# Optimization experiments

Measured on AMD Instinct MI355X. Metric: run time of the kernel, lower is better.

## Reference

```python
import jax, jax.numpy as jnp
import numpy as np
import math

B, QL, HID = 4, 4, 4096          # batch, speculative q_len, hidden_size
NH, NKV, HD = 32, 8, 128         # attention heads, kv heads, head_dim
GROUPS = NH // NKV               # GQA repeat factor = 4
PRIOR = 4096                     # cached (prior) KV length
THETA = 1.0e6                    # Mixtral rope_theta


def setup_inputs() -> dict:
    key = jax.random.key(0)
    ks = jax.random.split(key, 7)
    hidden_states = jax.random.normal(ks[0], (B, QL, HID), jnp.float32)
    past_k = jax.random.normal(ks[1], (B, NKV, PRIOR, HD), jnp.float32)
    past_v = jax.random.normal(ks[2], (B, NKV, PRIOR, HD), jnp.float32)
    wq = jax.random.normal(ks[3], (HID, NH * HD), jnp.float32) * 0.02
    wk = jax.random.normal(ks[4], (HID, NKV * HD), jnp.float32) * 0.02
    wv = jax.random.normal(ks[5], (HID, NKV * HD), jnp.float32) * 0.02
    wo = jax.random.normal(ks[6], (NH * HD, HID), jnp.float32) * 0.02
    # prior mask: all cached positions visible
    attention_mask = jnp.ones((B, 1, QL, PRIOR), dtype=bool)
    # active mask: causal over the speculative window
    active_mask = jnp.broadcast_to(jnp.tril(jnp.ones((QL, QL), dtype=bool)), (B, 1, QL, QL))
    position_ids = jnp.broadcast_to(PRIOR + jnp.arange(QL, dtype=jnp.int64), (B, QL))
    return {"hidden_states": hidden_states, "past_k": past_k, "past_v": past_v,
            "wq": wq, "wk": wk, "wv": wv, "wo": wo,
            "attention_mask": attention_mask, "active_mask": active_mask,
            "position_ids": position_ids}


def _rotate_half(x):
    x1, x2 = jnp.split(x, 2, axis=-1)
    return jnp.concatenate([-x2, x1], axis=-1)


def _rope_cos_sin(position_ids):
    inv_freq = 1.0 / (THETA ** (jnp.arange(0, HD, 2, dtype=jnp.float32) / HD))  # [HD/2]
    freqs = position_ids.astype(jnp.float32)[..., None] * inv_freq              # [B,QL,HD/2]
    emb = jnp.concatenate([freqs, freqs], axis=-1)                              # [B,QL,HD]
    return jnp.cos(emb)[:, None], jnp.sin(emb)[:, None]                          # [B,1,QL,HD]


def reference(hidden_states, past_k, past_v, wq, wk, wv, wo,
              attention_mask, active_mask, position_ids):
    # fused QKV projection (no bias in Mixtral)
    q = (hidden_states @ wq).reshape(B, QL, NH, HD).transpose(0, 2, 1, 3)   # [B,NH,QL,HD]
    k = (hidden_states @ wk).reshape(B, QL, NKV, HD).transpose(0, 2, 1, 3)  # [B,NKV,QL,HD]
    v = (hidden_states @ wv).reshape(B, QL, NKV, HD).transpose(0, 2, 1, 3)
    # RoPE on Q and active K
    cos, sin = _rope_cos_sin(position_ids)
    q = q * cos + _rotate_half(q) * sin
    k = k * cos + _rotate_half(k) * sin
    # GQA repeat_kv
    k_prior = jnp.repeat(past_k, GROUPS, axis=1)  # [B,NH,PRIOR,HD]
    v_prior = jnp.repeat(past_v, GROUPS, axis=1)
    k_active = jnp.repeat(k, GROUPS, axis=1)      # [B,NH,QL,HD]
    v_active = jnp.repeat(v, GROUPS, axis=1)
    scale = 1.0 / math.sqrt(HD)
    neg = jnp.finfo(jnp.float32).min
    prior_scores = jnp.einsum('bhqd,bhkd->bhqk', q, k_prior) * scale
    prior_scores = jnp.where(attention_mask, prior_scores, neg)
    active_scores = jnp.einsum('bhqd,bhkd->bhqk', q, k_active) * scale
    active_scores = jnp.where(active_mask, active_scores, neg)   # is_speculation=True
    # decomposed softmax: shared max and shared divisor across prior/active
    max_score = jnp.maximum(prior_scores.max(-1, keepdims=True),
                            active_scores.max(-1, keepdims=True))
    prior_exp = jnp.exp(prior_scores - max_score)
    active_exp = jnp.exp(active_scores - max_score)
    divisor = prior_exp.sum(-1, keepdims=True) + active_exp.sum(-1, keepdims=True)
    attn = (jnp.einsum('bhqk,bhkd->bhqd', prior_exp / divisor, v_prior) +
            jnp.einsum('bhqk,bhkd->bhqd', active_exp / divisor, v_active))
    attn = attn.transpose(0, 2, 1, 3).reshape(B, QL, NH * HD)
    return attn @ wo
```

## Files before the change

kernel.cpp:

```cpp
#include <hip/hip_runtime.h>
#include <math.h>

#define NROWS 16
#define NCOLS 6144
#define HID   4096
#define NKV   8
#define HD    128
#define PRIOR 4096
#define NCH   16
#define CHUNK 256
#define SUB   64
#define KC1   128
#define NKC   32

__device__ __forceinline__ void gemm16x2_chunk(const float* __restrict__ A, int lda,
                                               const float* __restrict__ Wp, int ldw,
                                               int k0, float acc[NROWS][2])
{
#pragma unroll 2
    for (int kk = 0; kk < KC1; kk += 4) {
        const int kg = k0 + kk;
        const float2 w0 = *(const float2*)(Wp + (size_t)(kg + 0) * ldw);
        const float2 w1 = *(const float2*)(Wp + (size_t)(kg + 1) * ldw);
        const float2 w2 = *(const float2*)(Wp + (size_t)(kg + 2) * ldw);
        const float2 w3 = *(const float2*)(Wp + (size_t)(kg + 3) * ldw);
#pragma unroll
        for (int m = 0; m < NROWS; m++) {
            const float4 h4 = *(const float4*)(A + m * lda + kg);
            acc[m][0] = fmaf(h4.x, w0.x, fmaf(h4.y, w1.x, fmaf(h4.z, w2.x, fmaf(h4.w, w3.x, acc[m][0]))));
            acc[m][1] = fmaf(h4.x, w0.y, fmaf(h4.y, w1.y, fmaf(h4.z, w2.y, fmaf(h4.w, w3.y, acc[m][1]))));
        }
    }
}

__global__ __launch_bounds__(256)
void k_qkv_partial(const float* __restrict__ hid,
                   const float* __restrict__ wq,
                   const float* __restrict__ wk,
                   const float* __restrict__ wv,
                   float* __restrict__ part)
{
    const int t   = threadIdx.x;
    const int col = blockIdx.x * 512 + t * 2;
    const int kc  = blockIdx.y;
    const float* w; int wn, wcol;
    if (col < 4096)      { w = wq; wn = 4096; wcol = col; }
    else if (col < 5120) { w = wk; wn = 1024; wcol = col - 4096; }
    else                 { w = wv; wn = 1024; wcol = col - 5120; }

    float acc[NROWS][2];
#pragma unroll
    for (int m = 0; m < NROWS; m++) { acc[m][0] = 0.f; acc[m][1] = 0.f; }

    gemm16x2_chunk(hid, HID, w + wcol, wn, kc * KC1, acc);

    float* po = part + (size_t)kc * (NROWS * NCOLS) + col;
#pragma unroll
    for (int m = 0; m < NROWS; m++)
        *(float2*)(po + m * NCOLS) = make_float2(acc[m][0], acc[m][1]);
}

__global__ __launch_bounds__(256)
void k_reduce_rope(const float* __restrict__ part, float* __restrict__ qkv)
{
    const int tid = blockIdx.x * 256 + threadIdx.x;
    const double L64 = 0.21586735246819178;

    if (tid < 32768) {
        const int d = tid & 63, h = (tid >> 6) & 31, r = tid >> 11;
        const int c1 = h * HD + d;
        float s1 = 0.f, s2 = 0.f;
        for (int c = 0; c < NKC; c++) {
            const float* p = part + (size_t)c * (NROWS * NCOLS) + r * NCOLS + c1;
            s1 += p[0]; s2 += p[64];
        }
        const double ang = (double)(PRIOR + (r & 3)) * exp(-(double)d * L64);
        double sv, cv; sincos(ang, &sv, &cv);
        const float cf = (float)cv, sf = (float)sv, sc = 0.08838834764831845f;
        qkv[r * NCOLS + c1]      = (s1 * cf - s2 * sf) * sc;
        qkv[r * NCOLS + c1 + 64] = (s2 * cf + s1 * sf) * sc;
    } else if (tid < 40960) {
        const int idx = tid - 32768;
        const int d = idx & 63, kh = (idx >> 6) & 7, r = idx >> 9;
        const int c1 = 4096 + kh * HD + d;
        float s1 = 0.f, s2 = 0.f;
        for (int c = 0; c < NKC; c++) {
            const float* p = part + (size_t)c * (NROWS * NCOLS) + r * NCOLS + c1;
            s1 += p[0]; s2 += p[64];
        }
        const double ang = (double)(PRIOR + (r & 3)) * exp(-(double)d * L64);
        double sv, cv; sincos(ang, &sv, &cv);
        const float cf = (float)cv, sf = (float)sv;
        qkv[r * NCOLS + c1]      = s1 * cf - s2 * sf;
        qkv[r * NCOLS + c1 + 64] = s2 * cf + s1 * sf;
    } else {
        const int idx = tid - 40960;
        const int n = idx & 1023, r = idx >> 10;
        const int c1 = 5120 + n;
        float s = 0.f;
        for (int c = 0; c < NKC; c++)
            s += part[(size_t)c * (NROWS * NCOLS) + r * NCOLS + c1];
        qkv[r * NCOLS + c1] = s;
    }
}

__global__ __launch_bounds__(256)
void k_attn_prior(const float* __restrict__ qkv,
                  const float* __restrict__ pk,
                  const float* __restrict__ pv,
                  float* __restrict__ part3)
{
    const int chunk = blockIdx.x, kvh = blockIdx.y, b = blockIdx.z;
    const int t = threadIdx.x;

    __shared__ float qT[128][16];
    __shared__ float kT[128][64];
    __shared__ float sS[4][16][68];
    __shared__ float pP[64][20];
    __shared__ float mS[16], lS[16], aS[16];

    for (int i = t; i < 2048; i += 256) {
        const int qi = i & 15, d = i >> 4;
        const int ql = qi & 3, g = qi >> 2;
        qT[d][qi] = qkv[(b * 4 + ql) * NCOLS + (kvh * 4 + g) * HD + d];
    }
    if (t < 16) { mS[t] = -INFINITY; lS[t] = 0.f; }

    const int dt = t & 31, rp = t >> 5;
    float o[2][4] = {{0.f,0.f,0.f,0.f},{0.f,0.f,0.f,0.f}};
    const int h = t >> 6, qt = (t >> 4) & 3, kt = t & 15;
    const size_t kvoff = ((size_t)(b * NKV + kvh) * PRIOR + (size_t)chunk * CHUNK) * HD;
    const float* kbase = pk + kvoff;
    const float* vbase = pv + kvoff;
    __syncthreads();

    for (int st = 0; st < CHUNK / SUB; st++) {
        {
            const int key = t & 63, hh = t >> 6;
            const float* kr = kbase + (st * SUB + key) * HD;
#pragma unroll
            for (int i = 0; i < 8; i++) {
                const int dq = hh * 8 + i;
                const float4 k4 = *(const float4*)(kr + dq * 4);
                kT[dq * 4 + 0][key] = k4.x;
                kT[dq * 4 + 1][key] = k4.y;
                kT[dq * 4 + 2][key] = k4.z;
                kT[dq * 4 + 3][key] = k4.w;
            }
        }
        __syncthreads();
        {
            float a[4][4] = {{0.f,0.f,0.f,0.f},{0.f,0.f,0.f,0.f},{0.f,0.f,0.f,0.f},{0.f,0.f,0.f,0.f}};
#pragma unroll 8
            for (int dd = 0; dd < 32; dd++) {
                const int d = h * 32 + dd;
                const float4 q4 = *(const float4*)(&qT[d][qt * 4]);
                const float4 k4 = *(const float4*)(&kT[d][kt * 4]);
                a[0][0]=fmaf(q4.x,k4.x,a[0][0]); a[0][1]=fmaf(q4.x,k4.y,a[0][1]); a[0][2]=fmaf(q4.x,k4.z,a[0][2]); a[0][3]=fmaf(q4.x,k4.w,a[0][3]);
                a[1][0]=fmaf(q4.y,k4.x,a[1][0]); a[1][1]=fmaf(q4.y,k4.y,a[1][1]); a[1][2]=fmaf(q4.y,k4.z,a[1][2]); a[1][3]=fmaf(q4.y,k4.w,a[1][3]);
                a[2][0]=fmaf(q4.z,k4.x,a[2][0]); a[2][1]=fmaf(q4.z,k4.y,a[2][1]); a[2][2]=fmaf(q4.z,k4.z,a[2][2]); a[2][3]=fmaf(q4.z,k4.w,a[2][3]);
                a[3][0]=fmaf(q4.w,k4.x,a[3][0]); a[3][1]=fmaf(q4.w,k4.y,a[3][1]); a[3][2]=fmaf(q4.w,k4.z,a[3][2]); a[3][3]=fmaf(q4.w,k4.w,a[3][3]);
            }
#pragma unroll
            for (int i = 0; i < 4; i++)
                *(float4*)(&sS[h][qt * 4 + i][kt * 4]) = make_float4(a[i][0], a[i][1], a[i][2], a[i][3]);
        }
        __syncthreads();
        {
            const int w = t >> 6, lane = t & 63;
            float sv[4], mx[4], mn[4], sm[4];
#pragma unroll
            for (int i = 0; i < 4; i++) {
                const int r = w * 4 + i;
                sv[i] = sS[0][r][lane] + sS[1][r][lane] + sS[2][r][lane] + sS[3][r][lane];
                mx[i] = sv[i];
            }
            for (int off = 32; off; off >>= 1) {
#pragma unroll
                for (int i = 0; i < 4; i++) mx[i] = fmaxf(mx[i], __shfl_xor(mx[i], off));
            }
#pragma unroll
            for (int i = 0; i < 4; i++) {
                const int r = w * 4 + i;
                mn[i] = fmaxf(mS[r], mx[i]);
                const float p = __expf(sv[i] - mn[i]);
                pP[lane][r] = p;
                sm[i] = p;
            }
            for (int off = 32; off; off >>= 1) {
#pragma unroll
                for (int i = 0; i < 4; i++) sm[i] += __shfl_xor(sm[i], off);
            }
            if (lane == 0) {
#pragma unroll
                for (int i = 0; i < 4; i++) {
                    const int r = w * 4 + i;
                    const float al = __expf(mS[r] - mn[i]);
                    aS[r] = al;
                    lS[r] = lS[r] * al + sm[i];
                    mS[r] = mn[i];
                }
            }
        }
        __syncthreads();
        {
            const float a0 = aS[2 * rp], a1 = aS[2 * rp + 1];
#pragma unroll
            for (int j = 0; j < 4; j++) { o[0][j] *= a0; o[1][j] *= a1; }
            const float* vs = vbase + st * SUB * HD + dt * 4;
#pragma unroll 8
            for (int key = 0; key < SUB; key++) {
                const float4 v4 = *(const float4*)(vs + key * HD);
                const float p0 = pP[key][2 * rp], p1 = pP[key][2 * rp + 1];
                o[0][0]=fmaf(p0,v4.x,o[0][0]); o[0][1]=fmaf(p0,v4.y,o[0][1]); o[0][2]=fmaf(p0,v4.z,o[0][2]); o[0][3]=fmaf(p0,v4.w,o[0][3]);
                o[1][0]=fmaf(p1,v4.x,o[1][0]); o[1][1]=fmaf(p1,v4.y,o[1][1]); o[1][2]=fmaf(p1,v4.z,o[1][2]); o[1][3]=fmaf(p1,v4.w,o[1][3]);
            }
        }
    }

    float* pout = part3 + ((size_t)((b * NKV + kvh) * NCH + chunk)) * 2080;
    if (t < 16) { pout[t] = mS[t]; pout[16 + t] = lS[t]; }
#pragma unroll
    for (int j = 0; j < 2; j++) {
        const int r = 2 * rp + j;
        *(float4*)(pout + 32 + r * HD + dt * 4) = make_float4(o[j][0], o[j][1], o[j][2], o[j][3]);
    }
}

__global__ __launch_bounds__(256)
void k_combine(const float* __restrict__ qkv,
               const float* __restrict__ part3,
               float* __restrict__ attn)
{
    const int kvh = blockIdx.x & 7, b = blockIdx.x >> 3;
    const int t = threadIdx.x;
    __shared__ float qL[16][132], kA[4][132], vA[4][132];
    __shared__ float mC[NCH][16], lC[NCH][16], fC[NCH][16];
    __shared__ float sAct[16][4], pA[16][4], invL[16];

    for (int i = t; i < 2048; i += 256) {
        const int qi = i & 15, d = i >> 4, ql = qi & 3, g = qi >> 2;
        qL[qi][d] = qkv[(b * 4 + ql) * NCOLS + (kvh * 4 + g) * HD + d];
    }
    for (int i = t; i < 512; i += 256) {
        const int k = i & 3, d = i >> 2;
        kA[k][d] = qkv[(b * 4 + k) * NCOLS + 4096 + kvh * HD + d];
        vA[k][d] = qkv[(b * 4 + k) * NCOLS + 5120 + kvh * HD + d];
    }
    const float* p3 = part3 + (size_t)(b * NKV + kvh) * NCH * 2080;
    for (int i = t; i < NCH * 16; i += 256) {
        const int c = i >> 4, r = i & 15;
        mC[c][r] = p3[c * 2080 + r];
        lC[c][r] = p3[c * 2080 + 16 + r];
    }
    __syncthreads();

    if (t < 64) {
        const int r = t >> 2, k = t & 3;
        float s = 0.f;
        for (int d = 0; d < HD; d++) s = fmaf(qL[r][d], kA[k][d], s);
        sAct[r][k] = s;
    }
    __syncthreads();
    if (t < 16) {
        const int r = t, ql = r & 3;
        float M = -INFINITY;
        for (int c = 0; c < NCH; c++) M = fmaxf(M, mC[c][r]);
        for (int k = 0; k <= ql; k++) M = fmaxf(M, sAct[r][k]);
        float l = 0.f;
        for (int c = 0; c < NCH; c++) {
            const float f = __expf(mC[c][r] - M);
            fC[c][r] = f;
            l = fmaf(f, lC[c][r], l);
        }
#pragma unroll
        for (int k = 0; k < 4; k++) {
            const float p = (k <= ql) ? __expf(sAct[r][k] - M) : 0.f;
            pA[r][k] = p; l += p;
        }
        invL[r] = 1.f / l;
    }
    __syncthreads();

    const int dt = t & 31, rp = t >> 5;
    float o[2][4] = {{0.f,0.f,0.f,0.f},{0.f,0.f,0.f,0.f}};
    for (int c = 0; c < NCH; c++) {
        const float* pa = p3 + c * 2080 + 32 + dt * 4;
#pragma unroll
        for (int j = 0; j < 2; j++) {
            const int r = 2 * rp + j;
            const float f = fC[c][r];
            const float4 a4 = *(const float4*)(pa + r * HD);
            o[j][0]=fmaf(f,a4.x,o[j][0]); o[j][1]=fmaf(f,a4.y,o[j][1]); o[j][2]=fmaf(f,a4.z,o[j][2]); o[j][3]=fmaf(f,a4.w,o[j][3]);
        }
    }
#pragma unroll
    for (int k = 0; k < 4; k++) {
        const float4 v4 = *(const float4*)(&vA[k][dt * 4]);
#pragma unroll
        for (int j = 0; j < 2; j++) {
            const float p = pA[2 * rp + j][k];
            o[j][0]=fmaf(p,v4.x,o[j][0]); o[j][1]=fmaf(p,v4.y,o[j][1]); o[j][2]=fmaf(p,v4.z,o[j][2]); o[j][3]=fmaf(p,v4.w,o[j][3]);
        }
    }
#pragma unroll
    for (int j = 0; j < 2; j++) {
        const int r = 2 * rp + j, ql = r & 3, g = r >> 2;
        const float il = invL[r];
        *(float4*)(attn + (b * 4 + ql) * HID + (kvh * 4 + g) * HD + dt * 4) =
            make_float4(o[j][0] * il, o[j][1] * il, o[j][2] * il, o[j][3] * il);
    }
}

__global__ __launch_bounds__(256)
void k_out_partial(const float* __restrict__ attn,
                   const float* __restrict__ wo,
                   float* __restrict__ part)
{
    const int t = threadIdx.x;
    const int col = blockIdx.x * 512 + t * 2;
    const int kc = blockIdx.y;

    float acc[NROWS][2];
#pragma unroll
    for (int m = 0; m < NROWS; m++) { acc[m][0] = 0.f; acc[m][1] = 0.f; }

    gemm16x2_chunk(attn, HID, wo + col, HID, kc * KC1, acc);

    float* po = part + (size_t)kc * (NROWS * HID) + col;
#pragma unroll
    for (int m = 0; m < NROWS; m++)
        *(float2*)(po + m * HID) = make_float2(acc[m][0], acc[m][1]);
}

__global__ __launch_bounds__(256)
void k_out_reduce(const float* __restrict__ part, float* __restrict__ out)
{
    const int tid = blockIdx.x * 256 + threadIdx.x;
    float s = 0.f;
    for (int c = 0; c < NKC; c++) s += part[(size_t)c * (NROWS * HID) + tid];
    out[tid] = s;
}

extern "C" void kernel_launch(void* const* d_in, const int* in_sizes, int n_in,
                              void* d_out, int out_size, void* d_ws, size_t ws_size,
                              hipStream_t stream)
{
    (void)in_sizes; (void)n_in; (void)out_size; (void)ws_size;
    const float* hid = (const float*)d_in[0];
    const float* pk  = (const float*)d_in[1];
    const float* pv  = (const float*)d_in[2];
    const float* wq  = (const float*)d_in[3];
    const float* wk  = (const float*)d_in[4];
    const float* wv  = (const float*)d_in[5];
    const float* wo  = (const float*)d_in[6];
    float* out = (float*)d_out;
    float* ws  = (float*)d_ws;

    float* P1   = ws;
    float* P5   = ws;
    float* attn = ws + 2097152;
    float* qkv  = ws + 3145728;
    float* P3   = ws + 3145728 + 98304;

    k_qkv_partial<<<dim3(12, NKC), 256, 0, stream>>>(hid, wq, wk, wv, P1);
    k_reduce_rope<<<224, 256, 0, stream>>>(P1, qkv);
    k_attn_prior<<<dim3(NCH, NKV, 4), 256, 0, stream>>>(qkv, pk, pv, P3);
    k_combine<<<32, 256, 0, stream>>>(qkv, P3, attn);
    k_out_partial<<<dim3(8, NKC), 256, 0, stream>>>(attn, wo, P5);
    k_out_reduce<<<256, 256, 0, stream>>>(P5, out);
}
```

Baseline: 324.6 us.

## Rework GEMVs with LDS-staged activations, restructure attention and combine parallelism

Stages the activation rows in LDS for the QKV and output-projection GEMVs, with one column per thread and twice as many blocks. Rewrites the prior-attention kernel: KV chunks are halved and their count doubled, each thread now owns one key for QK and one dim for PV, and running max and sum live in registers. Splits the combine kernel per head group and vectorises the output reduction. It also reuses the workspace by aliasing P3 with P1 and P5. The aim is more parallelism and fewer redundant global activation reads, at the cost of narrower weight loads and Q values re-read from global memory in the dot product.

```diff
diff --git a/kernel.cpp b/kernel.cpp
--- a/kernel.cpp
+++ b/kernel.cpp
@@ -7,31 +7,11 @@
 #define NKV   8
 #define HD    128
 #define PRIOR 4096
-#define NCH   16
-#define CHUNK 256
+#define NCH   32
+#define CHUNK 128
 #define SUB   64
 #define KC1   128
 #define NKC   32
-
-__device__ __forceinline__ void gemm16x2_chunk(const float* __restrict__ A, int lda,
-                                               const float* __restrict__ Wp, int ldw,
-                                               int k0, float acc[NROWS][2])
-{
-#pragma unroll 2
-    for (int kk = 0; kk < KC1; kk += 4) {
-        const int kg = k0 + kk;
-        const float2 w0 = *(const float2*)(Wp + (size_t)(kg + 0) * ldw);
-        const float2 w1 = *(const float2*)(Wp + (size_t)(kg + 1) * ldw);
-        const float2 w2 = *(const float2*)(Wp + (size_t)(kg + 2) * ldw);
-        const float2 w3 = *(const float2*)(Wp + (size_t)(kg + 3) * ldw);
-#pragma unroll
-        for (int m = 0; m < NROWS; m++) {
-            const float4 h4 = *(const float4*)(A + m * lda + kg);
-            acc[m][0] = fmaf(h4.x, w0.x, fmaf(h4.y, w1.x, fmaf(h4.z, w2.x, fmaf(h4.w, w3.x, acc[m][0]))));
-            acc[m][1] = fmaf(h4.x, w0.y, fmaf(h4.y, w1.y, fmaf(h4.z, w2.y, fmaf(h4.w, w3.y, acc[m][1]))));
-        }
-    }
-}
 
 __global__ __launch_bounds__(256)
 void k_qkv_partial(const float* __restrict__ hid,
@@ -41,23 +21,39 @@
                    float* __restrict__ part)
 {
     const int t   = threadIdx.x;
-    const int col = blockIdx.x * 512 + t * 2;
+    const int col = blockIdx.x * 256 + t;
     const int kc  = blockIdx.y;
+    const int k0  = kc * KC1;
+    __shared__ float sA[NROWS][KC1];
+    for (int i = t; i < NROWS * KC1; i += 256) {
+        const int r = i >> 7, kk = i & 127;
+        sA[r][kk] = hid[(size_t)r * HID + k0 + kk];
+    }
     const float* w; int wn, wcol;
     if (col < 4096)      { w = wq; wn = 4096; wcol = col; }
     else if (col < 5120) { w = wk; wn = 1024; wcol = col - 4096; }
     else                 { w = wv; wn = 1024; wcol = col - 5120; }
-
-    float acc[NROWS][2];
-#pragma unroll
-    for (int m = 0; m < NROWS; m++) { acc[m][0] = 0.f; acc[m][1] = 0.f; }
-
-    gemm16x2_chunk(hid, HID, w + wcol, wn, kc * KC1, acc);
-
+    const float* wp = w + wcol + (size_t)k0 * wn;
+    __syncthreads();
+
+    float acc[NROWS];
+#pragma unroll
+    for (int m = 0; m < NROWS; m++) acc[m] = 0.f;
+#pragma unroll 2
+    for (int kk = 0; kk < KC1; kk += 4) {
+        const float w0 = wp[(size_t)(kk + 0) * wn];
+        const float w1 = wp[(size_t)(kk + 1) * wn];
+        const float w2 = wp[(size_t)(kk + 2) * wn];
+        const float w3 = wp[(size_t)(kk + 3) * wn];
+#pragma unroll
+        for (int m = 0; m < NROWS; m++) {
+            const float4 h4 = *(const float4*)(&sA[m][kk]);
+            acc[m] = fmaf(h4.x, w0, fmaf(h4.y, w1, fmaf(h4.z, w2, fmaf(h4.w, w3, acc[m]))));
+        }
+    }
     float* po = part + (size_t)kc * (NROWS * NCOLS) + col;
 #pragma unroll
-    for (int m = 0; m < NROWS; m++)
-        *(float2*)(po + m * NCOLS) = make_float2(acc[m][0], acc[m][1]);
+    for (int m = 0; m < NROWS; m++) po[(size_t)m * NCOLS] = acc[m];
 }
 
 __global__ __launch_bounds__(256)
@@ -104,7 +100,7 @@
     }
 }
 
-__global__ __launch_bounds__(256)
+__global__ __launch_bounds__(256, 4)
 void k_attn_prior(const float* __restrict__ qkv,
                   const float* __restrict__ pk,
                   const float* __restrict__ pv,
@@ -113,118 +109,104 @@
     const int chunk = blockIdx.x, kvh = blockIdx.y, b = blockIdx.z;
     const int t = threadIdx.x;
 
-    __shared__ float qT[128][16];
-    __shared__ float kT[128][64];
-    __shared__ float sS[4][16][68];
-    __shared__ float pP[64][20];
-    __shared__ float mS[16], lS[16], aS[16];
-
-    for (int i = t; i < 2048; i += 256) {
-        const int qi = i & 15, d = i >> 4;
-        const int ql = qi & 3, g = qi >> 2;
-        qT[d][qi] = qkv[(b * 4 + ql) * NCOLS + (kvh * 4 + g) * HD + d];
-    }
-    if (t < 16) { mS[t] = -INFINITY; lS[t] = 0.f; }
-
-    const int dt = t & 31, rp = t >> 5;
-    float o[2][4] = {{0.f,0.f,0.f,0.f},{0.f,0.f,0.f,0.f}};
-    const int h = t >> 6, qt = (t >> 4) & 3, kt = t & 15;
+    __shared__ float kT[SUB][132];
+    __shared__ float pP[SUB][16];
+    __shared__ float aS[16];
+
+    const int key = t & 63;
+    const int qg  = t >> 6;
+    const int dpv = t & 127;
+    const int rh  = t >> 7;
+
     const size_t kvoff = ((size_t)(b * NKV + kvh) * PRIOR + (size_t)chunk * CHUNK) * HD;
     const float* kbase = pk + kvoff;
     const float* vbase = pv + kvoff;
-    __syncthreads();
+
+    const float* qr[4];
+#pragma unroll
+    for (int i = 0; i < 4; i++)
+        qr[i] = qkv + (size_t)(b * 4 + i) * NCOLS + (kvh * 4 + qg) * HD;
+
+    float m_r[4], l_r[4];
+#pragma unroll
+    for (int i = 0; i < 4; i++) { m_r[i] = -INFINITY; l_r[i] = 0.f; }
+    float o[8] = {0.f,0.f,0.f,0.f,0.f,0.f,0.f,0.f};
 
     for (int st = 0; st < CHUNK / SUB; st++) {
-        {
-            const int key = t & 63, hh = t >> 6;
-            const float* kr = kbase + (st * SUB + key) * HD;
-#pragma unroll
-            for (int i = 0; i < 8; i++) {
-                const int dq = hh * 8 + i;
-                const float4 k4 = *(const float4*)(kr + dq * 4);
-                kT[dq * 4 + 0][key] = k4.x;
-                kT[dq * 4 + 1][key] = k4.y;
-                kT[dq * 4 + 2][key] = k4.z;
-                kT[dq * 4 + 3][key] = k4.w;
-            }
+#pragma unroll
+        for (int p = 0; p < 8; p++) {
+            const int i = p * 256 + t;
+            const int kk = i >> 5, dl = (i & 31) * 4;
+            const float4 k4 = *(const float4*)(kbase + (size_t)(st * SUB + kk) * HD + dl);
+            *(float4*)(&kT[kk][dl]) = k4;
         }
         __syncthreads();
-        {
-            float a[4][4] = {{0.f,0.f,0.f,0.f},{0.f,0.f,0.f,0.f},{0.f,0.f,0.f,0.f},{0.f,0.f,0.f,0.f}};
+        float s0 = 0.f, s1 = 0.f, s2 = 0.f, s3 = 0.f;
+#pragma unroll 2
+        for (int d = 0; d < HD; d += 4) {
+            const float4 k4 = *(const float4*)(&kT[key][d]);
+            const float4 qa = *(const float4*)(qr[0] + d);
+            const float4 qb = *(const float4*)(qr[1] + d);
+            const float4 qc = *(const float4*)(qr[2] + d);
+            const float4 qd = *(const float4*)(qr[3] + d);
+            s0 = fmaf(qa.x,k4.x, fmaf(qa.y,k4.y, fmaf(qa.z,k4.z, fmaf(qa.w,k4.w, s0))));
+            s1 = fmaf(qb.x,k4.x, fmaf(qb.y,k4.y, fmaf(qb.z,k4.z, fmaf(qb.w,k4.w, s1))));
+            s2 = fmaf(qc.x,k4.x, fmaf(qc.y,k4.y, fmaf(qc.z,k4.z, fmaf(qc.w,k4.w, s2))));
+            s3 = fmaf(qd.x,k4.x, fmaf(qd.y,k4.y, fmaf(qd.z,k4.z, fmaf(qd.w,k4.w, s3))));
+        }
+        float sv[4] = {s0, s1, s2, s3};
+        float mx[4] = {s0, s1, s2, s3};
+        for (int off = 32; off; off >>= 1) {
+#pragma unroll
+            for (int i = 0; i < 4; i++) mx[i] = fmaxf(mx[i], __shfl_xor(mx[i], off));
+        }
+        float pr[4], sm[4], al[4];
+#pragma unroll
+        for (int i = 0; i < 4; i++) {
+            const float mn = fmaxf(m_r[i], mx[i]);
+            pr[i] = __expf(sv[i] - mn);
+            al[i] = __expf(m_r[i] - mn);
+            m_r[i] = mn;
+            sm[i] = pr[i];
+        }
+        *(float4*)(&pP[key][qg * 4]) = make_float4(pr[0], pr[1], pr[2], pr[3]);
+        for (int off = 32; off; off >>= 1) {
+#pragma unroll
+            for (int i = 0; i < 4; i++) sm[i] += __shfl_xor(sm[i], off);
+        }
+#pragma unroll
+        for (int i = 0; i < 4; i++) l_r[i] = l_r[i] * al[i] + sm[i];
+        if (key == 0) {
+#pragma unroll
+            for (int i = 0; i < 4; i++) aS[qg * 4 + i] = al[i];
+        }
+        __syncthreads();
+        float alv[8];
+#pragma unroll
+        for (int j = 0; j < 8; j++) alv[j] = aS[rh * 8 + j];
+#pragma unroll
+        for (int j = 0; j < 8; j++) o[j] *= alv[j];
+        const float* vs = vbase + (size_t)st * SUB * HD + dpv;
 #pragma unroll 8
-            for (int dd = 0; dd < 32; dd++) {
-                const int d = h * 32 + dd;
-                const float4 q4 = *(const float4*)(&qT[d][qt * 4]);
-                const float4 k4 = *(const float4*)(&kT[d][kt * 4]);
-                a[0][0]=fmaf(q4.x,k4.x,a[0][0]); a[0][1]=fmaf(q4.x,k4.y,a[0][1]); a[0][2]=fmaf(q4.x,k4.z,a[0][2]); a[0][3]=fmaf(q4.x,k4.w,a[0][3]);
-                a[1][0]=fmaf(q4.y,k4.x,a[1][0]); a[1][1]=fmaf(q4.y,k4.y,a[1][1]); a[1][2]=fmaf(q4.y,k4.z,a[1][2]); a[1][3]=fmaf(q4.y,k4.w,a[1][3]);
-                a[2][0]=fmaf(q4.z,k4.x,a[2][0]); a[2][1]=fmaf(q4.z,k4.y,a[2][1]); a[2][2]=fmaf(q4.z,k4.z,a[2][2]); a[2][3]=fmaf(q4.z,k4.w,a[2][3]);
-                a[3][0]=fmaf(q4.w,k4.x,a[3][0]); a[3][1]=fmaf(q4.w,k4.y,a[3][1]); a[3][2]=fmaf(q4.w,k4.z,a[3][2]); a[3][3]=fmaf(q4.w,k4.w,a[3][3]);
-            }
-#pragma unroll
-            for (int i = 0; i < 4; i++)
-                *(float4*)(&sS[h][qt * 4 + i][kt * 4]) = make_float4(a[i][0], a[i][1], a[i][2], a[i][3]);
+        for (int k2 = 0; k2 < SUB; k2++) {
+            const float v = vs[(size_t)k2 * HD];
+            const float4 pa = *(const float4*)(&pP[k2][rh * 8]);
+            const float4 pb = *(const float4*)(&pP[k2][rh * 8 + 4]);
+            o[0] = fmaf(pa.x, v, o[0]); o[1] = fmaf(pa.y, v, o[1]);
+            o[2] = fmaf(pa.z, v, o[2]); o[3] = fmaf(pa.w, v, o[3]);
+            o[4] = fmaf(pb.x, v, o[4]); o[5] = fmaf(pb.y, v, o[5]);
+            o[6] = fmaf(pb.z, v, o[6]); o[7] = fmaf(pb.w, v, o[7]);
         }
         __syncthreads();
-        {
-            const int w = t >> 6, lane = t & 63;
-            float sv[4], mx[4], mn[4], sm[4];
-#pragma unroll
-            for (int i = 0; i < 4; i++) {
-                const int r = w * 4 + i;
-                sv[i] = sS[0][r][lane] + sS[1][r][lane] + sS[2][r][lane] + sS[3][r][lane];
-                mx[i] = sv[i];
-            }
-            for (int off = 32; off; off >>= 1) {
-#pragma unroll
-                for (int i = 0; i < 4; i++) mx[i] = fmaxf(mx[i], __shfl_xor(mx[i], off));
-            }
-#pragma unroll
-            for (int i = 0; i < 4; i++) {
-                const int r = w * 4 + i;
-                mn[i] = fmaxf(mS[r], mx[i]);
-                const float p = __expf(sv[i] - mn[i]);
-                pP[lane][r] = p;
-                sm[i] = p;
-            }
-            for (int off = 32; off; off >>= 1) {
-#pragma unroll
-                for (int i = 0; i < 4; i++) sm[i] += __shfl_xor(sm[i], off);
-            }
-            if (lane == 0) {
-#pragma unroll
-                for (int i = 0; i < 4; i++) {
-                    const int r = w * 4 + i;
-                    const float al = __expf(mS[r] - mn[i]);
-                    aS[r] = al;
-                    lS[r] = lS[r] * al + sm[i];
-                    mS[r] = mn[i];
-                }
-            }
-        }
-        __syncthreads();
-        {
-            const float a0 = aS[2 * rp], a1 = aS[2 * rp + 1];
-#pragma unroll
-            for (int j = 0; j < 4; j++) { o[0][j] *= a0; o[1][j] *= a1; }
-            const float* vs = vbase + st * SUB * HD + dt * 4;
-#pragma unroll 8
-            for (int key = 0; key < SUB; key++) {
-                const float4 v4 = *(const float4*)(vs + key * HD);
-                const float p0 = pP[key][2 * rp], p1 = pP[key][2 * rp + 1];
-                o[0][0]=fmaf(p0,v4.x,o[0][0]); o[0][1]=fmaf(p0,v4.y,o[0][1]); o[0][2]=fmaf(p0,v4.z,o[0][2]); o[0][3]=fmaf(p0,v4.w,o[0][3]);
-                o[1][0]=fmaf(p1,v4.x,o[1][0]); o[1][1]=fmaf(p1,v4.y,o[1][1]); o[1][2]=fmaf(p1,v4.z,o[1][2]); o[1][3]=fmaf(p1,v4.w,o[1][3]);
-            }
-        }
-    }
-
-    float* pout = part3 + ((size_t)((b * NKV + kvh) * NCH + chunk)) * 2080;
-    if (t < 16) { pout[t] = mS[t]; pout[16 + t] = lS[t]; }
-#pragma unroll
-    for (int j = 0; j < 2; j++) {
-        const int r = 2 * rp + j;
-        *(float4*)(pout + 32 + r * HD + dt * 4) = make_float4(o[j][0], o[j][1], o[j][2], o[j][3]);
-    }
+    }
+    float* pout = part3 + (size_t)((b * NKV + kvh) * NCH + chunk) * 2080;
+    if (key == 0) {
+#pragma unroll
+        for (int i = 0; i < 4; i++) { pout[qg * 4 + i] = m_r[i]; pout[16 + qg * 4 + i] = l_r[i]; }
+    }
+#pragma unroll
+    for (int j = 0; j < 8; j++)
+        pout[32 + (rh * 8 + j) * HD + dpv] = o[j];
 }
 
 __global__ __launch_bounds__(256)
@@ -232,84 +214,69 @@
                const float* __restrict__ part3,
                float* __restrict__ attn)
 {
-    const int kvh = blockIdx.x & 7, b = blockIdx.x >> 3;
+    const int g = blockIdx.x & 3, kvh = (blockIdx.x >> 2) & 7, b = blockIdx.x >> 5;
     const int t = threadIdx.x;
-    __shared__ float qL[16][132], kA[4][132], vA[4][132];
-    __shared__ float mC[NCH][16], lC[NCH][16], fC[NCH][16];
-    __shared__ float sAct[16][4], pA[16][4], invL[16];
-
-    for (int i = t; i < 2048; i += 256) {
-        const int qi = i & 15, d = i >> 4, ql = qi & 3, g = qi >> 2;
-        qL[qi][d] = qkv[(b * 4 + ql) * NCOLS + (kvh * 4 + g) * HD + d];
-    }
+    __shared__ float qL[4][128], kA[4][128], vA[4][128];
+    __shared__ float mC[NCH][4], lC[NCH][4], fC[NCH][4];
+    __shared__ float sAct[4][4], pA[4][4], invL[4];
+
     for (int i = t; i < 512; i += 256) {
-        const int k = i & 3, d = i >> 2;
-        kA[k][d] = qkv[(b * 4 + k) * NCOLS + 4096 + kvh * HD + d];
-        vA[k][d] = qkv[(b * 4 + k) * NCOLS + 5120 + kvh * HD + d];
+        const int ql = i >> 7, d = i & 127;
+        qL[ql][d] = qkv[(size_t)(b * 4 + ql) * NCOLS + (kvh * 4 + g) * HD + d];
+        kA[ql][d] = qkv[(size_t)(b * 4 + ql) * NCOLS + 4096 + kvh * HD + d];
+        vA[ql][d] = qkv[(size_t)(b * 4 + ql) * NCOLS + 5120 + kvh * HD + d];
     }
     const float* p3 = part3 + (size_t)(b * NKV + kvh) * NCH * 2080;
-    for (int i = t; i < NCH * 16; i += 256) {
-        const int c = i >> 4, r = i & 15;
-        mC[c][r] = p3[c * 2080 + r];
-        lC[c][r] = p3[c * 2080 + 16 + r];
-    }
-    __syncthreads();
-
-    if (t < 64) {
-        const int r = t >> 2, k = t & 3;
+    for (int i = t; i < NCH * 4; i += 256) {
+        const int c = i >> 2, lr = i & 3;
+        mC[c][lr] = p3[c * 2080 + g * 4 + lr];
+        lC[c][lr] = p3[c * 2080 + 16 + g * 4 + lr];
+    }
+    __syncthreads();
+    if (t < 16) {
+        const int lr = t >> 2, k = t & 3;
         float s = 0.f;
-        for (int d = 0; d < HD; d++) s = fmaf(qL[r][d], kA[k][d], s);
-        sAct[r][k] = s;
-    }
-    __syncthreads();
-    if (t < 16) {
-        const int r = t, ql = r & 3;
+        for (int d = 0; d < HD; d++) s = fmaf(qL[lr][d], kA[k][d], s);
+        sAct[lr][k] = s;
+    }
+    __syncthreads();
+    if (t < 4) {
+        const int lr = t;
         float M = -INFINITY;
-        for (int c = 0; c < NCH; c++) M = fmaxf(M, mC[c][r]);
-        for (int k = 0; k <= ql; k++) M = fmaxf(M, sAct[r][k]);
+        for (int c = 0; c < NCH; c++) M = fmaxf(M, mC[c][lr]);
+        for (int k = 0; k <= lr; k++) M = fmaxf(M, sAct[lr][k]);
         float l = 0.f;
         for (int c = 0; c < NCH; c++) {
-            const float f = __expf(mC[c][r] - M);
-            fC[c][r] = f;
-            l = fmaf(f, lC[c][r], l);
+            const float f = __expf(mC[c][lr] - M);
+            fC[c][lr] = f;
+            l = fmaf(f, lC[c][lr], l);
         }
 #pragma unroll
         for (int k = 0; k < 4; k++) {
-            const float p = (k <= ql) ? __expf(sAct[r][k] - M) : 0.f;
-            pA[r][k] = p; l += p;
-        }
-        invL[r] = 1.f / l;
-    }
-    __syncthreads();
-
-    const int dt = t & 31, rp = t >> 5;
-    float o[2][4] = {{0.f,0.f,0.f,0.f},{0.f,0.f,0.f,0.f}};
+            const float p = (k <= lr) ? __expf(sAct[lr][k] - M) : 0.f;
+            pA[lr][k] = p; l += p;
+        }
+        invL[lr] = 1.f / l;
+    }
+    __syncthreads();
+
+    const int d = t & 127, hr = t >> 7;
+    const int lr0 = hr * 2, lr1 = hr * 2 + 1;
+    float o0 = 0.f, o1 = 0.f;
     for (int c = 0; c < NCH; c++) {
-        const float* pa = p3 + c * 2080 + 32 + dt * 4;
-#pragma unroll
-        for (int j = 0; j < 2; j++) {
-            const int r = 2 * rp + j;
-            const float f = fC[c][r];
-            const float4 a4 = *(const float4*)(pa + r * HD);
-            o[j][0]=fmaf(f,a4.x,o[j][0]); o[j][1]=fmaf(f,a4.y,o[j][1]); o[j][2]=fmaf(f,a4.z,o[j][2]); o[j][3]=fmaf(f,a4.w,o[j][3]);
-        }
+        const float f0 = fC[c][lr0], f1 = fC[c][lr1];
+        const float* pa = p3 + c * 2080 + 32 + (g * 4 + lr0) * HD + d;
+        o0 = fmaf(f0, pa[0],  o0);
+        o1 = fmaf(f1, pa[HD], o1);
     }
 #pragma unroll
     for (int k = 0; k < 4; k++) {
-        const float4 v4 = *(const float4*)(&vA[k][dt * 4]);
-#pragma unroll
-        for (int j = 0; j < 2; j++) {
-            const float p = pA[2 * rp + j][k];
-            o[j][0]=fmaf(p,v4.x,o[j][0]); o[j][1]=fmaf(p,v4.y,o[j][1]); o[j][2]=fmaf(p,v4.z,o[j][2]); o[j][3]=fmaf(p,v4.w,o[j][3]);
-        }
-    }
-#pragma unroll
-    for (int j = 0; j < 2; j++) {
-        const int r = 2 * rp + j, ql = r & 3, g = r >> 2;
-        const float il = invL[r];
-        *(float4*)(attn + (b * 4 + ql) * HID + (kvh * 4 + g) * HD + dt * 4) =
-            make_float4(o[j][0] * il, o[j][1] * il, o[j][2] * il, o[j][3] * il);
-    }
+        const float v = vA[k][d];
+        o0 = fmaf(pA[lr0][k], v, o0);
+        o1 = fmaf(pA[lr1][k], v, o1);
+    }
+    attn[(size_t)(b * 4 + lr0) * HID + (kvh * 4 + g) * HD + d] = o0 * invL[lr0];
+    attn[(size_t)(b * 4 + lr1) * HID + (kvh * 4 + g) * HD + d] = o1 * invL[lr1];
 }
 
 __global__ __launch_bounds__(256)
@@ -318,28 +285,48 @@
                    float* __restrict__ part)
 {
     const int t = threadIdx.x;
-    const int col = blockIdx.x * 512 + t * 2;
+    const int col = blockIdx.x * 256 + t;
     const int kc = blockIdx.y;
-
-    float acc[NROWS][2];
-#pragma unroll
-    for (int m = 0; m < NROWS; m++) { acc[m][0] = 0.f; acc[m][1] = 0.f; }
-
-    gemm16x2_chunk(attn, HID, wo + col, HID, kc * KC1, acc);
-
+    const int k0 = kc * KC1;
+    __shared__ float sA[NROWS][KC1];
+    for (int i = t; i < NROWS * KC1; i += 256) {
+        const int r = i >> 7, kk = i & 127;
+        sA[r][kk] = attn[(size_t)r * HID + k0 + kk];
+    }
+    const float* wp = wo + col + (size_t)k0 * HID;
+    __syncthreads();
+
+    float acc[NROWS];
+#pragma unroll
+    for (int m = 0; m < NROWS; m++) acc[m] = 0.f;
+#pragma unroll 2
+    for (int kk = 0; kk < KC1; kk += 4) {
+        const float w0 = wp[(size_t)(kk + 0) * HID];
+        const float w1 = wp[(size_t)(kk + 1) * HID];
+        const float w2 = wp[(size_t)(kk + 2) * HID];
+        const float w3 = wp[(size_t)(kk + 3) * HID];
+#pragma unroll
+        for (int m = 0; m < NROWS; m++) {
+            const float4 h4 = *(const float4*)(&sA[m][kk]);
+            acc[m] = fmaf(h4.x, w0, fmaf(h4.y, w1, fmaf(h4.z, w2, fmaf(h4.w, w3, acc[m]))));
+        }
+    }
     float* po = part + (size_t)kc * (NROWS * HID) + col;
 #pragma unroll
-    for (int m = 0; m < NROWS; m++)
-        *(float2*)(po + m * HID) = make_float2(acc[m][0], acc[m][1]);
+    for (int m = 0; m < NROWS; m++) po[(size_t)m * HID] = acc[m];
 }
 
 __global__ __launch_bounds__(256)
 void k_out_reduce(const float* __restrict__ part, float* __restrict__ out)
 {
     const int tid = blockIdx.x * 256 + threadIdx.x;
-    float s = 0.f;
-    for (int c = 0; c < NKC; c++) s += part[(size_t)c * (NROWS * HID) + tid];
-    out[tid] = s;
+    const float* p = part + (size_t)tid * 4;
+    float4 s = make_float4(0.f, 0.f, 0.f, 0.f);
+    for (int c = 0; c < NKC; c++) {
+        const float4 a = *(const float4*)(p + (size_t)c * (NROWS * HID));
+        s.x += a.x; s.y += a.y; s.z += a.z; s.w += a.w;
+    }
+    *(float4*)(out + (size_t)tid * 4) = s;
 }
 
 extern "C" void kernel_launch(void* const* d_in, const int* in_sizes, int n_in,
@@ -358,15 +345,15 @@
     float* ws  = (float*)d_ws;
 
     float* P1   = ws;
+    float* P3   = ws;
     float* P5   = ws;
-    float* attn = ws + 2097152;
     float* qkv  = ws + 3145728;
-    float* P3   = ws + 3145728 + 98304;
-
-    k_qkv_partial<<<dim3(12, NKC), 256, 0, stream>>>(hid, wq, wk, wv, P1);
+    float* attn = ws + 3244032;
+
+    k_qkv_partial<<<dim3(24, NKC), 256, 0, stream>>>(hid, wq, wk, wv, P1);
     k_reduce_rope<<<224, 256, 0, stream>>>(P1, qkv);
     k_attn_prior<<<dim3(NCH, NKV, 4), 256, 0, stream>>>(qkv, pk, pv, P3);
-    k_combine<<<32, 256, 0, stream>>>(qkv, P3, attn);
-    k_out_partial<<<dim3(8, NKC), 256, 0, stream>>>(attn, wo, P5);
-    k_out_reduce<<<256, 256, 0, stream>>>(P5, out);
-}
+    k_combine<<<128, 256, 0, stream>>>(qkv, P3, attn);
+    k_out_partial<<<dim3(16, NKC), 256, 0, stream>>>(attn, wo, P5);
+    k_out_reduce<<<64, 256, 0, stream>>>(P5, out);
+}
```

Result: slower. 368.0 us (+13.4%).
